# Kernel optimization log

Measured on AMD Instinct MI355X. Metric: run time of the kernel, lower is better.

The kernel has to match this reference:

```python
import jax, jax.numpy as jnp
import numpy as np

N = 100_000          # nodes
E = 3_200_000        # edges (avg degree 32)
DIMS = [6, 20, 15, 10, 5, 2]


def setup_inputs() -> dict:
    key = jax.random.key(0)
    ks = jax.random.split(key, 3 + 2 * 5)
    inp = {
        "x": jax.random.normal(ks[0], (N, DIMS[0]), jnp.float32),
        "edge_index": jax.random.randint(ks[1], (2, E), 0, N, jnp.int32),
        "edge_weight": jax.random.uniform(ks[2], (E,), jnp.float32),
    }
    for i in range(5):
        din, dout = DIMS[i], DIMS[i + 1]
        s = 1.0 / np.sqrt(din)
        inp[f"w_rel{i}"] = jax.random.normal(ks[3 + 2 * i], (din, dout), jnp.float32) * s
        inp[f"b_rel{i}"] = jnp.zeros((dout,), jnp.float32)
        inp[f"w_root{i}"] = jax.random.normal(ks[4 + 2 * i], (din, dout), jnp.float32) * s
    return inp


def _graph_conv(x, src, dst, w, W_rel, b_rel, W_root):
    # PyG GraphConv: lin_rel(scatter_add(w_e * x_src)) + lin_root(x)
    msg = x[src] * w[:, None]                                  # [E, din]
    agg = jax.ops.segment_sum(msg, dst, num_segments=N)        # [N, din]
    return agg @ W_rel + b_rel + x @ W_root                    # [N, dout]


def reference(x, edge_index, edge_weight,
              w_rel0, b_rel0, w_root0,
              w_rel1, b_rel1, w_root1,
              w_rel2, b_rel2, w_root2,
              w_rel3, b_rel3, w_root3,
              w_rel4, b_rel4, w_root4):
    src, dst = edge_index[0], edge_index[1]
    layers = [
        (w_rel0, b_rel0, w_root0),
        (w_rel1, b_rel1, w_root1),
        (w_rel2, b_rel2, w_root2),
        (w_rel3, b_rel3, w_root3),
        (w_rel4, b_rel4, w_root4),
    ]
    for W_rel, b_rel, W_root in layers:
        x = jax.nn.relu(_graph_conv(x, src, dst, edge_weight, W_rel, b_rel, W_root))
    return jax.nn.softmax(x, axis=1)
```

## Files before the change

### kernel.cpp

```cpp
#include <hip/hip_runtime.h>
#include <hip/hip_fp16.h>
#include <stdint.h>

#define N_NODES 100000
#define N_EDGES 3200000
#define BN      64
#define NB      1563
#define NCH_H   1024
#define CH_H    (N_EDGES / NCH_H)
#define CPL     (NCH_H / 64)
#define PAD_PER 98
#define NCH_S   256
#define CH_S    (N_EDGES / NCH_S)
#define BS1     1024
#define S1_IT   ((CH_S + BS1 - 1) / BS1)
#define S2_CAP  2560
#define BLOCK   256
#define W_SCALE 32767.0f
#define W_INV   (1.0f / 32767.0f)

__global__ void hist_kernel(const int* __restrict__ dst, int* __restrict__ hist_g,
                            const float* __restrict__ x, __half* __restrict__ xpad) {
    __shared__ int h[NB];
    for (int b = threadIdx.x; b < NB; b += BLOCK) h[b] = 0;
    {
        int i = blockIdx.x * PAD_PER + threadIdx.x;
        if (threadIdx.x < PAD_PER && i < N_NODES) {
            const float* xr = x + (size_t)i * 6;
            __half2 hh[4];
            hh[0] = __halves2half2(__float2half(xr[0]), __float2half(xr[1]));
            hh[1] = __halves2half2(__float2half(xr[2]), __float2half(xr[3]));
            hh[2] = __halves2half2(__float2half(xr[4]), __float2half(xr[5]));
            hh[3] = __halves2half2(__float2half(0.f),   __float2half(0.f));
            *(uint4*)(xpad + (size_t)i * 8) = *(uint4*)hh;
        }
    }
    __syncthreads();
    const int c  = blockIdx.x;
    const int k0 = c * CH_H;
    for (int k = threadIdx.x; k < CH_H; k += BLOCK)
        atomicAdd(&h[dst[k0 + k] >> 6], 1);
    __syncthreads();
    for (int b = threadIdx.x; b < NB; b += BLOCK)
        hist_g[c * NB + b] = h[b];
}

__global__ void chunkscan_kernel(const int* __restrict__ hist_g,
                                 int* __restrict__ off_g, int* __restrict__ tot) {
    int w    = (blockIdx.x * blockDim.x + threadIdx.x) >> 6;
    int lane = threadIdx.x & 63;
    if (w >= NB) return;
    int v[CPL];
    int ls = 0;
    const int cbase = lane * CPL;
    #pragma unroll
    for (int i = 0; i < CPL; ++i) { v[i] = hist_g[(cbase + i) * NB + w]; ls += v[i]; }
    int run = ls;
    #pragma unroll
    for (int d = 1; d < 64; d <<= 1) {
        int u = __shfl_up(run, d);
        if (lane >= d) run += u;
    }
    int acc = run - ls;
    #pragma unroll
    for (int i = 0; i < CPL; ++i) { off_g[(cbase + i) * NB + w] = acc; acc += v[i]; }
    if (lane == 63) tot[w] = acc;
}

#define SCAN_T   1024
#define SCAN_PER 2
__global__ void scan_kernel(const int* __restrict__ cnt, int* __restrict__ bstart) {
    __shared__ int part[SCAN_T];
    int t = threadIdx.x;
    int local[SCAN_PER];
    int s = 0;
    #pragma unroll
    for (int i = 0; i < SCAN_PER; ++i) {
        int idx = t * SCAN_PER + i;
        int v = (idx < NB) ? cnt[idx] : 0;
        local[i] = s;
        s += v;
    }
    part[t] = s;
    __syncthreads();
    for (int off = 1; off < SCAN_T; off <<= 1) {
        int v = (t >= off) ? part[t - off] : 0;
        __syncthreads();
        part[t] += v;
        __syncthreads();
    }
    int excl = part[t] - s;
    #pragma unroll
    for (int i = 0; i < SCAN_PER; ++i) {
        int idx = t * SCAN_PER + i;
        if (idx < NB) bstart[idx] = excl + local[i];
    }
}

__global__ void __launch_bounds__(BS1)
scatter1_kernel(const int* __restrict__ src, const int* __restrict__ dst,
                const float* __restrict__ w,
                const int* __restrict__ bstart, const int* __restrict__ off_g,
                uint32_t* __restrict__ recA, uint8_t* __restrict__ recD) {
    __shared__ uint32_t stage[CH_S];
    __shared__ int h[NB];
    __shared__ int delta[NB];
    __shared__ int wtot[BS1 / 64];

    const int c  = blockIdx.x;
    const int k0 = c * CH_S;
    const int t  = threadIdx.x;

    for (int b = t; b < NB; b += BS1) h[b] = 0;
    __syncthreads();
    int dstv[S1_IT];
    int nit = 0;
    for (int k = t; k < CH_S; k += BS1, ++nit) {
        int d = dst[k0 + k];
        dstv[nit] = d;
        atomicAdd(&h[d >> 6], 1);
    }
    __syncthreads();

    {
        const int base = t * 2;
        int v[2], ls = 0;
        #pragma unroll
        for (int i = 0; i < 2; ++i) {
            int idx = base + i;
            v[i] = (idx < NB) ? h[idx] : 0;
            ls += v[i];
        }
        int lane = t & 63, wv = t >> 6;
        int run = ls;
        #pragma unroll
        for (int d = 1; d < 64; d <<= 1) {
            int u = __shfl_up(run, d);
            if (lane >= d) run += u;
        }
        if (lane == 63) wtot[wv] = run;
        __syncthreads();
        int wexcl = 0;
        for (int i = 0; i < wv; ++i) wexcl += wtot[i];
        int excl = wexcl + run - ls;
        #pragma unroll
        for (int i = 0; i < 2; ++i) {
            int idx = base + i;
            if (idx < NB) {
                int gb = bstart[idx] + off_g[(size_t)(4 * c) * NB + idx];
                h[idx]     = excl;
                delta[idx] = gb - excl;
                excl += v[i];
            }
        }
    }
    __syncthreads();

    nit = 0;
    for (int k = t; k < CH_S; k += BS1, ++nit) {
        int d = dstv[nit];
        int b = d >> 6;
        int pos = atomicAdd(&h[b], 1);
        stage[pos] = (uint32_t)k | ((uint32_t)(d & 63) << 14) | ((uint32_t)b << 20);
    }
    __syncthreads();

    for (int i = t; i < CH_S; i += BS1) {
        uint32_t sv = stage[i];
        int le = sv & 0x3FFF;
        int dl = (sv >> 14) & 0x3F;
        int b  = sv >> 20;
        int e  = k0 + le;
        uint32_t w15 = (uint32_t)__float2uint_rn(w[e] * W_SCALE);
        int pos = delta[b] + i;
        recA[pos] = (uint32_t)src[e] | (w15 << 17);
        recD[pos] = (uint8_t)dl;
    }
}

__global__ void scatter2_kernel(const uint32_t* __restrict__ recA,
                                const uint8_t* __restrict__ recD,
                                const int* __restrict__ bstart, const int* __restrict__ tot,
                                uint32_t* __restrict__ rec2,
                                int* __restrict__ row_start, int* __restrict__ cnt) {
    __shared__ int h[BN];
    __shared__ int cur[BN];
    __shared__ uint32_t stage[S2_CAP];
    const int b  = blockIdx.x;
    const int s0 = bstart[b];
    const int n  = tot[b];
    if (threadIdx.x < BN) h[threadIdx.x] = 0;
    __syncthreads();
    for (int k = threadIdx.x; k < n; k += BLOCK)
        atomicAdd(&h[recD[s0 + k]], 1);
    __syncthreads();
    if (threadIdx.x < BN) {
        int v = h[threadIdx.x];
        int run = v;
        #pragma unroll
        for (int d = 1; d < 64; d <<= 1) {
            int u = __shfl_up(run, d);
            if (threadIdx.x >= d) run += u;
        }
        int excl = run - v;
        cur[threadIdx.x] = excl;
        int node = b * BN + threadIdx.x;
        if (node < N_NODES) { row_start[node] = s0 + excl; cnt[node] = v; }
    }
    __syncthreads();
    for (int k = threadIdx.x; k < n; k += BLOCK) {
        uint32_t ra = recA[s0 + k];
        int dl = recD[s0 + k];
        int pos = atomicAdd(&cur[dl], 1);
        if (pos < S2_CAP) stage[pos] = ra;
        else              rec2[s0 + pos] = ra;
    }
    __syncthreads();
    for (int i = threadIdx.x; i < n && i < S2_CAP; i += BLOCK)
        rec2[s0 + i] = stage[i];
}

__global__ void layer0_kernel(const __half* __restrict__ xpad,
                              const uint32_t* __restrict__ rec,
                              const int* __restrict__ row_start, const int* __restrict__ cnt,
                              const float* __restrict__ wrel0, const float* __restrict__ brel0,
                              const float* __restrict__ wroot0,
                              const float* __restrict__ wrel1, const float* __restrict__ brel1,
                              const float* __restrict__ wroot1,
                              __half* __restrict__ pn, float* __restrict__ oinitn) {
    __shared__ float s_wrel0[6 * 20], s_wroot0[6 * 20], s_b0[20];
    __shared__ float s_wrel1[20 * 15], s_wroot1[20 * 15], s_b1[15];
    for (int t = threadIdx.x; t < 120; t += BLOCK) {
        s_wrel0[t]  = wrel0[t];
        s_wroot0[t] = wroot0[t];
    }
    for (int t = threadIdx.x; t < 300; t += BLOCK) {
        s_wrel1[t]  = wrel1[t];
        s_wroot1[t] = wroot1[t];
    }
    if (threadIdx.x < 20) s_b0[threadIdx.x] = brel0[threadIdx.x];
    else if (threadIdx.x >= 32 && threadIdx.x < 47) s_b1[threadIdx.x - 32] = brel1[threadIdx.x - 32];
    __syncthreads();

    int t = blockIdx.x * blockDim.x + threadIdx.x;
    int node = t >> 3;
    int q    = t & 7;

    float agg[6] = {0.f, 0.f, 0.f, 0.f, 0.f, 0.f};
    const int s = row_start[node];
    const int e = s + cnt[node];
    for (int k = s + q; k < e; k += 8) {
        uint32_t r = rec[k];
        float w = (float)(r >> 17) * W_INV;
        uint4 raw = *(const uint4*)(xpad + (size_t)(r & 0x1FFFF) * 8);
        const __half2* h = (const __half2*)&raw;
        agg[0] += w * __low2float(h[0]);  agg[1] += w * __high2float(h[0]);
        agg[2] += w * __low2float(h[1]);  agg[3] += w * __high2float(h[1]);
        agg[4] += w * __low2float(h[2]);  agg[5] += w * __high2float(h[2]);
    }
    #pragma unroll
    for (int i = 0; i < 6; ++i) {
        agg[i] += __shfl_xor(agg[i], 1);
        agg[i] += __shfl_xor(agg[i], 2);
        agg[i] += __shfl_xor(agg[i], 4);
    }
    uint4 raws = *(const uint4*)(xpad + (size_t)node * 8);
    const __half2* hs = (const __half2*)&raws;
    float xv[6] = { __low2float(hs[0]), __high2float(hs[0]),
                    __low2float(hs[1]), __high2float(hs[1]),
                    __low2float(hs[2]), __high2float(hs[2]) };

    float ov[20];
    #pragma unroll
    for (int j = 0; j < 20; ++j) {
        float o = s_b0[j];
        #pragma unroll
        for (int i = 0; i < 6; ++i)
            o += agg[i] * s_wrel0[i * 20 + j] + xv[i] * s_wroot0[i * 20 + j];
        ov[j] = fmaxf(o, 0.f);
    }

    {
        float pk[2] = {0.f, 0.f};
        #pragma unroll
        for (int kk = 0; kk < 2; ++kk) {
            int k = 2 * q + kk;
            if (k < 15) {
                float sacc = 0.f;
                #pragma unroll
                for (int j = 0; j < 20; ++j) sacc += ov[j] * s_wrel1[j * 15 + k];
                pk[kk] = sacc;
            }
        }
        ((__half2*)(pn + (size_t)node * 16))[q] =
            __halves2half2(__float2half(pk[0]), __float2half(pk[1]));
    }
    #pragma unroll
    for (int kk = 0; kk < 2; ++kk) {
        int k = q + kk * 8;
        if (k < 15) {
            float sacc = s_b1[k];
            #pragma unroll
            for (int j = 0; j < 20; ++j) sacc += ov[j] * s_wroot1[j * 15 + k];
            oinitn[(size_t)node * 15 + k] = sacc;
        }
    }
}

template<int DOUT, int SPH, int NDOUT, int NSPH, bool LAST>
__global__ void gather_kernel(const __half* __restrict__ p, const float* __restrict__ oinit,
                              const uint32_t* __restrict__ rec,
                              const int* __restrict__ row_start, const int* __restrict__ cnt,
                              const float* __restrict__ wrel_n, const float* __restrict__ brel_n,
                              const float* __restrict__ wroot_n,
                              __half* __restrict__ pn, float* __restrict__ oinitn,
                              float* __restrict__ out) {
    __shared__ float s_wrel[LAST ? 1 : DOUT * NDOUT];
    __shared__ float s_wroot[LAST ? 1 : DOUT * NDOUT];
    __shared__ float s_b[LAST ? 1 : (NDOUT > 0 ? NDOUT : 1)];
    if constexpr (!LAST) {
        for (int t = threadIdx.x; t < DOUT * NDOUT; t += BLOCK) {
            s_wrel[t]  = wrel_n[t];
            s_wroot[t] = wroot_n[t];
        }
        if (threadIdx.x < NDOUT) s_b[threadIdx.x] = brel_n[threadIdx.x];
        __syncthreads();
    }

    int t = blockIdx.x * blockDim.x + threadIdx.x;
    int node = t >> 3;
    int q    = t & 7;

    float af[SPH];
    #pragma unroll
    for (int i = 0; i < SPH; ++i) af[i] = 0.f;

    const int s = row_start[node];
    const int e = s + cnt[node];
    for (int k = s + q; k < e; k += 8) {
        uint32_t r = rec[k];
        float w = (float)(r >> 17) * W_INV;
        const __half* ps = p + (size_t)(r & 0x1FFFF) * SPH;
        if constexpr (SPH >= 8) {
            #pragma unroll
            for (int v = 0; v < SPH / 8; ++v) {
                uint4 raw = ((const uint4*)ps)[v];
                const __half2* h = (const __half2*)&raw;
                #pragma unroll
                for (int jj = 0; jj < 4; ++jj) {
                    af[v * 8 + 2 * jj]     += w * __low2float(h[jj]);
                    af[v * 8 + 2 * jj + 1] += w * __high2float(h[jj]);
                }
            }
        } else {
            uint32_t raw = *(const uint32_t*)ps;
            __half2 h = *(const __half2*)&raw;
            af[0] += w * __low2float(h);
            af[1] += w * __high2float(h);
        }
    }
    #pragma unroll
    for (int i = 0; i < SPH; ++i) {
        af[i] += __shfl_xor(af[i], 1);
        af[i] += __shfl_xor(af[i], 2);
        af[i] += __shfl_xor(af[i], 4);
    }

    if constexpr (LAST) {
        if (q == 0) {
            float o0 = af[0] + oinit[(size_t)node * 2 + 0];
            float o1 = af[1] + oinit[(size_t)node * 2 + 1];
            float m = fmaxf(o0, o1);
            float e0 = __expf(o0 - m), e1 = __expf(o1 - m);
            float inv = 1.f / (e0 + e1);
            out[(size_t)node * 2 + 0] = e0 * inv;
            out[(size_t)node * 2 + 1] = e1 * inv;
        }
    } else {
        float ov[DOUT];
        #pragma unroll
        for (int j = 0; j < DOUT; ++j)
            ov[j] = fmaxf(af[j] + oinit[(size_t)node * DOUT + j], 0.f);

        if (q < NSPH / 2) {
            float pk[2] = {0.f, 0.f};
            #pragma unroll
            for (int kk = 0; kk < 2; ++kk) {
                int k = 2 * q + kk;
                if (k < NDOUT) {
                    float sacc = 0.f;
                    #pragma unroll
                    for (int j = 0; j < DOUT; ++j) sacc += ov[j] * s_wrel[j * NDOUT + k];
                    pk[kk] = sacc;
                }
            }
            ((__half2*)(pn + (size_t)node * NSPH))[q] =
                __halves2half2(__float2half(pk[0]), __float2half(pk[1]));
        }
        #pragma unroll
        for (int kk = 0; kk < 2; ++kk) {
            int k = q + kk * 8;
            if (k < NDOUT) {
                float sacc = s_b[k];
                #pragma unroll
                for (int j = 0; j < DOUT; ++j) sacc += ov[j] * s_wroot[j * NDOUT + k];
                oinitn[(size_t)node * NDOUT + k] = sacc;
            }
        }
    }
}


extern "C" void kernel_launch(void* const* d_in, const int* in_sizes, int n_in,
                              void* d_out, int out_size, void* d_ws, size_t ws_size,
                              hipStream_t stream) {
    const float* x  = (const float*)d_in[0];
    const int*   ei = (const int*)d_in[1];
    const float* ew = (const float*)d_in[2];
    const float* wrel[5]  = { (const float*)d_in[3], (const float*)d_in[6],
                              (const float*)d_in[9], (const float*)d_in[12],
                              (const float*)d_in[15] };
    const float* brel[5]  = { (const float*)d_in[4], (const float*)d_in[7],
                              (const float*)d_in[10], (const float*)d_in[13],
                              (const float*)d_in[16] };
    const float* wroot[5] = { (const float*)d_in[5], (const float*)d_in[8],
                              (const float*)d_in[11], (const float*)d_in[14],
                              (const float*)d_in[17] };

    char* ws = (char*)d_ws;
    size_t off = 0;
    auto alloc = [&](size_t bytes) -> void* {
        void* ptr = ws + off;
        off += (bytes + 255) & ~(size_t)255;
        return ptr;
    };
    uint32_t* recA      = (uint32_t*)alloc((size_t)N_EDGES * 4);
    uint8_t*  recD      = (uint8_t*)alloc((size_t)N_EDGES);
    uint32_t* rec2      = (uint32_t*)alloc((size_t)N_EDGES * 4);
    __half*   xpad      = (__half*)alloc((size_t)N_NODES * 8 * 2);
    char*     regionB   = (char*)alloc((size_t)19 * 1024 * 1024);
    int*      hist_g    = (int*)regionB;
    int*      off_g     = (int*)(regionB + (size_t)NCH_H * NB * 4);
    __half*   pA        = (__half*)regionB;
    __half*   pB        = (__half*)(regionB + (size_t)4 * 1024 * 1024);
    float*    oA        = (float*)(regionB + (size_t)8 * 1024 * 1024);
    float*    oB        = (float*)(regionB + (size_t)14 * 1024 * 1024);
    int*      tot       = (int*)alloc((size_t)NB * 4);
    int*      bstart    = (int*)alloc((size_t)NB * 4);
    int*      row_start = (int*)alloc((size_t)N_NODES * 4);
    int*      cntb      = (int*)alloc((size_t)N_NODES * 4);
    float*    oB2       = (float*)alloc((size_t)N_NODES * 15 * 4);
    oB = oB2;

    const int* srcv = ei;
    const int* dstv = ei + N_EDGES;

    const int gN8 = (8 * N_NODES + BLOCK - 1) / BLOCK;

    hist_kernel     <<<NCH_H, BLOCK, 0, stream>>>(dstv, hist_g, x, xpad);
    chunkscan_kernel<<<(NB + 3) / 4, BLOCK, 0, stream>>>(hist_g, off_g, tot);
    scan_kernel     <<<1, SCAN_T, 0, stream>>>(tot, bstart);
    scatter1_kernel <<<NCH_S, BS1, 0, stream>>>(srcv, dstv, ew, bstart, off_g, recA, recD);
    scatter2_kernel <<<NB, BLOCK, 0, stream>>>(recA, recD, bstart, tot, rec2, row_start, cntb);

    layer0_kernel<<<gN8, BLOCK, 0, stream>>>(xpad, rec2, row_start, cntb,
                                             wrel[0], brel[0], wroot[0],
                                             wrel[1], brel[1], wroot[1], pA, oA);
    gather_kernel<15, 16, 10, 16, false><<<gN8, BLOCK, 0, stream>>>(
        pA, oA, rec2, row_start, cntb, wrel[2], brel[2], wroot[2], pB, oB, nullptr);
    gather_kernel<10, 16, 5, 8, false><<<gN8, BLOCK, 0, stream>>>(
        pB, oB, rec2, row_start, cntb, wrel[3], brel[3], wroot[3], pA, oA, nullptr);
    gather_kernel<5, 8, 2, 2, false><<<gN8, BLOCK, 0, stream>>>(
        pA, oA, rec2, row_start, cntb, wrel[4], brel[4], wroot[4], pB, oB, nullptr);
    gather_kernel<2, 2, 0, 0, true><<<gN8, BLOCK, 0, stream>>>(
        pB, oB, rec2, row_start, cntb, nullptr, nullptr, nullptr,
        nullptr, nullptr, (float*)d_out);
}
```

Measured before the change: 330.5 us.

## Pack scatter records as uint2, defer weight quantization, unroll gather loops 4x

The first scatter pass now writes one 8-byte record (src plus local dst in x, raw float weight in y) instead of separate 4-byte and 1-byte arrays. Weight quantization moves into the second scatter pass. The layer gather loops are unrolled four ways so that four independent record loads and four feature loads are in flight before accumulating, raising memory-level parallelism on the latency-bound gathers. The workspace layout is also reshuffled so activations alias the intermediate record buffer; the cost is more bytes written and read in the scatter stage and more registers in the gather kernels.

```diff
diff --git a/kernel.cpp b/kernel.cpp
--- a/kernel.cpp
+++ b/kernel.cpp
@@ -101,7 +101,7 @@
 scatter1_kernel(const int* __restrict__ src, const int* __restrict__ dst,
                 const float* __restrict__ w,
                 const int* __restrict__ bstart, const int* __restrict__ off_g,
-                uint32_t* __restrict__ recA, uint8_t* __restrict__ recD) {
+                uint2* __restrict__ rec1) {
     __shared__ uint32_t stage[CH_S];
     __shared__ int h[NB];
     __shared__ int delta[NB];
@@ -171,15 +171,14 @@
         int dl = (sv >> 14) & 0x3F;
         int b  = sv >> 20;
         int e  = k0 + le;
-        uint32_t w15 = (uint32_t)__float2uint_rn(w[e] * W_SCALE);
-        int pos = delta[b] + i;
-        recA[pos] = (uint32_t)src[e] | (w15 << 17);
-        recD[pos] = (uint8_t)dl;
-    }
-}
-
-__global__ void scatter2_kernel(const uint32_t* __restrict__ recA,
-                                const uint8_t* __restrict__ recD,
+        uint2 r;
+        r.x = (uint32_t)src[e] | ((uint32_t)dl << 17);
+        r.y = __float_as_uint(w[e]);
+        rec1[delta[b] + i] = r;
+    }
+}
+
+__global__ void scatter2_kernel(const uint2* __restrict__ rec1,
                                 const int* __restrict__ bstart, const int* __restrict__ tot,
                                 uint32_t* __restrict__ rec2,
                                 int* __restrict__ row_start, int* __restrict__ cnt) {
@@ -192,7 +191,7 @@
     if (threadIdx.x < BN) h[threadIdx.x] = 0;
     __syncthreads();
     for (int k = threadIdx.x; k < n; k += BLOCK)
-        atomicAdd(&h[recD[s0 + k]], 1);
+        atomicAdd(&h[rec1[s0 + k].x >> 17], 1);
     __syncthreads();
     if (threadIdx.x < BN) {
         int v = h[threadIdx.x];
@@ -209,11 +208,14 @@
     }
     __syncthreads();
     for (int k = threadIdx.x; k < n; k += BLOCK) {
-        uint32_t ra = recA[s0 + k];
-        int dl = recD[s0 + k];
+        uint2 r = rec1[s0 + k];
+        int dl = (int)(r.x >> 17);
+        float wv = __uint_as_float(r.y);
+        uint32_t w15 = (uint32_t)__float2uint_rn(wv * W_SCALE);
+        uint32_t r2 = (r.x & 0x1FFFF) | (w15 << 17);
         int pos = atomicAdd(&cur[dl], 1);
-        if (pos < S2_CAP) stage[pos] = ra;
-        else              rec2[s0 + pos] = ra;
+        if (pos < S2_CAP) stage[pos] = r2;
+        else              rec2[s0 + pos] = r2;
     }
     __syncthreads();
     for (int i = threadIdx.x; i < n && i < S2_CAP; i += BLOCK)
@@ -239,7 +241,7 @@
         s_wroot1[t] = wroot1[t];
     }
     if (threadIdx.x < 20) s_b0[threadIdx.x] = brel0[threadIdx.x];
-    else if (threadIdx.x >= 32 && threadIdx.x < 47) s_b1[threadIdx.x - 32] = brel1[threadIdx.x - 32];
+    if (threadIdx.x < 15) s_b1[threadIdx.x] = brel1[threadIdx.x];
     __syncthreads();
 
     int t = blockIdx.x * blockDim.x + threadIdx.x;
@@ -249,14 +251,28 @@
     float agg[6] = {0.f, 0.f, 0.f, 0.f, 0.f, 0.f};
     const int s = row_start[node];
     const int e = s + cnt[node];
-    for (int k = s + q; k < e; k += 8) {
-        uint32_t r = rec[k];
-        float w = (float)(r >> 17) * W_INV;
-        uint4 raw = *(const uint4*)(xpad + (size_t)(r & 0x1FFFF) * 8);
-        const __half2* h = (const __half2*)&raw;
-        agg[0] += w * __low2float(h[0]);  agg[1] += w * __high2float(h[0]);
-        agg[2] += w * __low2float(h[1]);  agg[3] += w * __high2float(h[1]);
-        agg[4] += w * __low2float(h[2]);  agg[5] += w * __high2float(h[2]);
+    for (int k = s + q; k < e; k += 32) {
+        uint32_t rv[4];
+        float    wv[4];
+        #pragma unroll
+        for (int u = 0; u < 4; ++u) {
+            int kk = k + 8 * u;
+            int kc = kk < e ? kk : (e - 1);
+            rv[u] = rec[kc];
+            wv[u] = kk < e ? (float)(rv[u] >> 17) * W_INV : 0.f;
+        }
+        uint4 raw[4];
+        #pragma unroll
+        for (int u = 0; u < 4; ++u)
+            raw[u] = *(const uint4*)(xpad + (size_t)(rv[u] & 0x1FFFF) * 8);
+        #pragma unroll
+        for (int u = 0; u < 4; ++u) {
+            const __half2* h = (const __half2*)&raw[u];
+            float w = wv[u];
+            agg[0] += w * __low2float(h[0]);  agg[1] += w * __high2float(h[0]);
+            agg[2] += w * __low2float(h[1]);  agg[3] += w * __high2float(h[1]);
+            agg[4] += w * __low2float(h[2]);  agg[5] += w * __high2float(h[2]);
+        }
     }
     #pragma unroll
     for (int i = 0; i < 6; ++i) {
@@ -337,26 +353,49 @@
 
     const int s = row_start[node];
     const int e = s + cnt[node];
-    for (int k = s + q; k < e; k += 8) {
-        uint32_t r = rec[k];
-        float w = (float)(r >> 17) * W_INV;
-        const __half* ps = p + (size_t)(r & 0x1FFFF) * SPH;
+    constexpr int NR = (SPH >= 8) ? SPH / 8 : 1;
+    for (int k = s + q; k < e; k += 32) {
+        uint32_t rv[4];
+        float    wv[4];
+        #pragma unroll
+        for (int u = 0; u < 4; ++u) {
+            int kk = k + 8 * u;
+            int kc = kk < e ? kk : (e - 1);
+            rv[u] = rec[kc];
+            wv[u] = kk < e ? (float)(rv[u] >> 17) * W_INV : 0.f;
+        }
         if constexpr (SPH >= 8) {
+            uint4 raw[4 * NR];
             #pragma unroll
-            for (int v = 0; v < SPH / 8; ++v) {
-                uint4 raw = ((const uint4*)ps)[v];
-                const __half2* h = (const __half2*)&raw;
+            for (int u = 0; u < 4; ++u) {
+                const uint4* ps = (const uint4*)(p + (size_t)(rv[u] & 0x1FFFF) * SPH);
                 #pragma unroll
-                for (int jj = 0; jj < 4; ++jj) {
-                    af[v * 8 + 2 * jj]     += w * __low2float(h[jj]);
-                    af[v * 8 + 2 * jj + 1] += w * __high2float(h[jj]);
+                for (int v = 0; v < NR; ++v) raw[u * NR + v] = ps[v];
+            }
+            #pragma unroll
+            for (int u = 0; u < 4; ++u) {
+                float w = wv[u];
+                #pragma unroll
+                for (int v = 0; v < NR; ++v) {
+                    const __half2* h = (const __half2*)&raw[u * NR + v];
+                    #pragma unroll
+                    for (int jj = 0; jj < 4; ++jj) {
+                        af[v * 8 + 2 * jj]     += w * __low2float(h[jj]);
+                        af[v * 8 + 2 * jj + 1] += w * __high2float(h[jj]);
+                    }
                 }
             }
         } else {
-            uint32_t raw = *(const uint32_t*)ps;
-            __half2 h = *(const __half2*)&raw;
-            af[0] += w * __low2float(h);
-            af[1] += w * __high2float(h);
+            uint32_t raw[4];
+            #pragma unroll
+            for (int u = 0; u < 4; ++u)
+                raw[u] = *(const uint32_t*)(p + (size_t)(rv[u] & 0x1FFFF) * SPH);
+            #pragma unroll
+            for (int u = 0; u < 4; ++u) {
+                __half2 h = *(const __half2*)&raw[u];
+                af[0] += wv[u] * __low2float(h);
+                af[1] += wv[u] * __high2float(h);
+            }
         }
     }
     #pragma unroll
@@ -434,23 +473,20 @@
         off += (bytes + 255) & ~(size_t)255;
         return ptr;
     };
-    uint32_t* recA      = (uint32_t*)alloc((size_t)N_EDGES * 4);
-    uint8_t*  recD      = (uint8_t*)alloc((size_t)N_EDGES);
+    char*     regionA   = (char*)alloc((size_t)N_EDGES * 8);
+    uint2*    rec1      = (uint2*)regionA;
+    __half*   pA        = (__half*)regionA;
+    __half*   pB        = (__half*)(regionA + (size_t)4  * 1024 * 1024);
+    float*    oA        = (float*)(regionA + (size_t)8  * 1024 * 1024);
+    float*    oB        = (float*)(regionA + (size_t)16 * 1024 * 1024);
     uint32_t* rec2      = (uint32_t*)alloc((size_t)N_EDGES * 4);
     __half*   xpad      = (__half*)alloc((size_t)N_NODES * 8 * 2);
-    char*     regionB   = (char*)alloc((size_t)19 * 1024 * 1024);
-    int*      hist_g    = (int*)regionB;
-    int*      off_g     = (int*)(regionB + (size_t)NCH_H * NB * 4);
-    __half*   pA        = (__half*)regionB;
-    __half*   pB        = (__half*)(regionB + (size_t)4 * 1024 * 1024);
-    float*    oA        = (float*)(regionB + (size_t)8 * 1024 * 1024);
-    float*    oB        = (float*)(regionB + (size_t)14 * 1024 * 1024);
+    int*      hist_g    = (int*)alloc((size_t)NCH_H * NB * 4);
+    int*      off_g     = (int*)alloc((size_t)NCH_H * NB * 4);
     int*      tot       = (int*)alloc((size_t)NB * 4);
     int*      bstart    = (int*)alloc((size_t)NB * 4);
     int*      row_start = (int*)alloc((size_t)N_NODES * 4);
     int*      cntb      = (int*)alloc((size_t)N_NODES * 4);
-    float*    oB2       = (float*)alloc((size_t)N_NODES * 15 * 4);
-    oB = oB2;
 
     const int* srcv = ei;
     const int* dstv = ei + N_EDGES;
@@ -460,8 +496,8 @@
     hist_kernel     <<<NCH_H, BLOCK, 0, stream>>>(dstv, hist_g, x, xpad);
     chunkscan_kernel<<<(NB + 3) / 4, BLOCK, 0, stream>>>(hist_g, off_g, tot);
     scan_kernel     <<<1, SCAN_T, 0, stream>>>(tot, bstart);
-    scatter1_kernel <<<NCH_S, BS1, 0, stream>>>(srcv, dstv, ew, bstart, off_g, recA, recD);
-    scatter2_kernel <<<NB, BLOCK, 0, stream>>>(recA, recD, bstart, tot, rec2, row_start, cntb);
+    scatter1_kernel <<<NCH_S, BS1, 0, stream>>>(srcv, dstv, ew, bstart, off_g, rec1);
+    scatter2_kernel <<<NB, BLOCK, 0, stream>>>(rec1, bstart, tot, rec2, row_start, cntb);
 
     layer0_kernel<<<gN8, BLOCK, 0, stream>>>(xpad, rec2, row_start, cntb,
                                              wrel[0], brel[0], wroot[0],
```

After: 322.7 us. -2.4%, faster.
